# Optimization experiments

Measured on AMD Instinct MI355X. Metric: run time of the kernel, lower is better.

Reference implementation:

```python
import jax, jax.numpy as jnp
import numpy as np

B, H, L, N = 8, 128, 4096, 64
EPS = 1e-7
LOG_DT_MIN, LOG_DT_MAX = np.log(0.001), np.log(0.1)


def setup_inputs() -> dict:
    key = jax.random.key(0)
    k_u, k_lre, k_w, k_step = jax.random.split(key, 4)
    u = jax.random.normal(k_u, (B, H, L), dtype=jnp.float32)
    # HiPPO-style diagonal init: Re(Lambda) < 0 for stability, Im(Lambda) = pi*n
    Lambda_re = -0.5 * jnp.ones((H, N), jnp.float32) \
        - 0.1 * jax.random.uniform(k_lre, (H, N), dtype=jnp.float32)
    Lambda_im = jnp.broadcast_to(jnp.pi * jnp.arange(N, dtype=jnp.float32), (H, N))
    # W stored as (real, imag) pairs, stddev sqrt(0.5) per the module's initializer
    W_ri = (0.5 ** 0.5) * jax.random.normal(k_w, (H, N, 2), dtype=jnp.float32)
    D = jnp.ones((H,), jnp.float32)
    # log_step ~ U[log(1e-3), log(1e-1)] per log_step_initializer
    log_step = jax.random.uniform(k_step, (H,), dtype=jnp.float32) \
        * (LOG_DT_MAX - LOG_DT_MIN) + LOG_DT_MIN
    return {"u": u, "Lambda_re": Lambda_re, "Lambda_im": Lambda_im,
            "W_ri": W_ri, "D": D, "log_step": log_step}


def _dss_kernel(W, Lambda, step, Lseq):
    # P[h,n,l] = step_h * Lambda_hn * l
    pos = jnp.arange(Lseq, dtype=jnp.float32)
    P = (step[:, None] * Lambda)[..., None] * pos          # [H,N,L] complex64
    # complex softmax over l, stabilized by the entry with largest real part
    idx = jnp.argmax(P.real, axis=-1)[..., None]           # [H,N,1]
    e = jnp.exp(P - jnp.take_along_axis(P, idx, axis=-1))
    s = jnp.sum(e, axis=-1, keepdims=True)
    S = e * (jnp.conj(s) / (s * jnp.conj(s) + EPS))        # e / s, eps-regularized
    return jnp.einsum('hn,hnl->hl', W / Lambda, S).real    # [H,L]


def reference(u, Lambda_re, Lambda_im, W_ri, D, log_step):
    Lambda = Lambda_re + 1j * Lambda_im                    # [H,N]
    W = W_ri[..., 0] + 1j * W_ri[..., 1]                   # [H,N]
    step = jnp.exp(log_step)                               # [H]
    Lseq = u.shape[-1]
    K = _dss_kernel(W, Lambda, step, Lseq)                 # [H,L]
    # FFT-based causal convolution, zero-padded to 2L
    n = 2 * Lseq
    uf = jnp.fft.rfft(u, n=n, axis=-1)                     # [B,H,L+1]
    Kf = jnp.fft.rfft(K, n=n, axis=-1)                     # [H,L+1]
    y = jnp.fft.irfft(uf * Kf[None], n=n, axis=-1)[..., :Lseq]
    return y + D[None, :, None] * u
```

## Files before the change

kernel.cpp:

```cpp
#include <hip/hip_runtime.h>
#include <math.h>

#define H_  128
#define N_  64
#define L_  4096
#define B_  8
#define LC  128
#define NCH 32

typedef _Float16 f16;
typedef _Float16 half8 __attribute__((ext_vector_type(8)));
typedef _Float16 f16x4 __attribute__((ext_vector_type(4)));
typedef _Float16 f16x2 __attribute__((ext_vector_type(2)));
typedef float    floatx4 __attribute__((ext_vector_type(4)));

#define WS_T 0
#define WS_G ((size_t)H_*LC*LC*2)
#define WS_M ((size_t)2*H_*LC*LC*2)
#define WS_Q ((size_t)3*H_*LC*LC*2)

__device__ __forceinline__ float fexp(float x) {
    return __builtin_amdgcn_exp2f(x * 1.4426950408889634f);
}
__device__ __forceinline__ void fcis(float th, float& cs, float& sn) {
    double rev = (double)th * 0.15915494309189535;
    rev -= floor(rev);
    const float r = (float)rev;
    sn = __builtin_amdgcn_sinf(r);
    cs = __builtin_amdgcn_cosf(r);
}
__device__ __forceinline__ void fcis64(double th, float& cs, float& sn) {
    double rev = th * 0.15915494309189535;
    rev -= floor(rev);
    const float r = (float)rev;
    sn = __builtin_amdgcn_sinf(r);
    cs = __builtin_amdgcn_cosf(r);
}

__device__ __forceinline__ void dss_consts(int h, int n,
    const float* __restrict__ Lre, const float* __restrict__ Lim,
    const float* __restrict__ Wri, const float* __restrict__ lstep,
    float& af, float& bf, float& crf, float& cif, float& qrf, float& qif)
{
    const float stepf = fexp(lstep[h]);
    const float a  = stepf * Lre[h*N_ + n];
    const float bp = stepf * Lim[h*N_ + n];
    const float em = fexp(a);
    float rcs, rsn; fcis(bp, rcs, rsn);
    const float rre = em*rcs, rim = em*rsn;
    const float eL = fexp(a * 4096.0f);
    float cL, sL; fcis64((double)bp * 4096.0, cL, sL);
    const float rLre = eL*cL, rLim = eL*sL;
    const float nre = 1.0f - rLre, nim = -rLim;
    const float dre = 1.0f - rre,  dim = -rim;
    const float dm  = dre*dre + dim*dim;
    const float sre = (nre*dre + nim*dim) / dm;
    const float sim = (nim*dre - nre*dim) / dm;
    const float wre = Wri[(h*N_ + n)*2 + 0];
    const float wim = Wri[(h*N_ + n)*2 + 1];
    const float lre = Lre[h*N_ + n], lim = Lim[h*N_ + n];
    const float lm  = lre*lre + lim*lim;
    const float wor = (wre*lre + wim*lim) / lm;
    const float woi = (wim*lre - wre*lim) / lm;
    const float sm  = sre*sre + sim*sim + 1e-7f;
    crf = (wor*sre + woi*sim) / sm;
    cif = (woi*sre - wor*sim) / sm;
    const float eC = fexp(a * 128.0f);
    float cC, sC; fcis64((double)bp * 128.0, cC, sC);
    qrf = eC*cC; qif = eC*sC;
    af = a; bf = bp;
}

__global__ __launch_bounds__(256)
void dss_prep(const float* __restrict__ Lre, const float* __restrict__ Lim,
              const float* __restrict__ Wri, const float* __restrict__ Dv,
              const float* __restrict__ lstep, char* __restrict__ ws)
{
    __shared__ float s_a[N_], s_b[N_], s_cr[N_], s_ci[N_];
    __shared__ float sKp[2][128];
    __shared__ float sK[128];
    const int h = blockIdx.x;
    const int which = blockIdx.y;
    const int t = threadIdx.x;

    if (t < N_) {
        float a, b, cr, ci, qr, qi;
        dss_consts(h, t, Lre, Lim, Wri, lstep, a, b, cr, ci, qr, qi);
        s_a[t] = a; s_b[t] = b; s_cr[t] = cr; s_ci[t] = ci;
        if (which == 0) {
            float* qg = (float*)(ws + WS_Q) + (size_t)h*N_*2;
            qg[2*t] = qr; qg[2*t+1] = qi;
        }
    }
    __syncthreads();

    if (which == 0) {
        const int lag = t & 127, hf = t >> 7;
        float acc = 0.f;
        #pragma unroll
        for (int m = 0; m < 32; ++m) {
            const int n = hf*32 + m;
            const float ex = fexp(s_a[n] * (float)lag);
            float cs, sn; fcis(s_b[n] * (float)lag, cs, sn);
            acc = fmaf(ex, s_cr[n]*cs - s_ci[n]*sn, acc);
        }
        sKp[hf][lag] = acc;
        __syncthreads();
        if (t < 128) {
            float kv = sKp[0][t] + sKp[1][t];
            if (t == 0) kv += Dv[h];
            sK[t] = kv;
        }
        __syncthreads();
        f16* Tg = (f16*)(ws + WS_T) + (size_t)h*LC*LC;
        #pragma unroll
        for (int i = 0; i < 8; ++i) {
            const int e8 = t + i*256;
            const int row = e8 >> 4, c0 = (e8 & 15) * 8;
            half8 pv;
            #pragma unroll
            for (int j = 0; j < 8; ++j) {
                const int col = c0 + j;
                pv[j] = (f16)((row >= col) ? sK[row - col] : 0.f);
            }
            *reinterpret_cast<half8*>(&Tg[row*LC + c0]) = pv;
        }
    } else if (which == 1) {
        f16* Gg = (f16*)(ws + WS_G) + (size_t)h*LC*LC;
        #pragma unroll
        for (int i = 0; i < 8; ++i) {
            const int e8 = t + i*256;
            const int row = e8 >> 4, c0 = (e8 & 15) * 8;
            const int m = row >> 1, im = row & 1;
            const float a = s_a[m], b = s_b[m];
            half8 pv;
            #pragma unroll
            for (int j = 0; j < 8; ++j) {
                const float p = (float)(127 - (c0 + j));
                const float ex = fexp(a * p);
                float cs, sn; fcis(b * p, cs, sn);
                pv[j] = (f16)(im ? ex*sn : ex*cs);
            }
            *reinterpret_cast<half8*>(&Gg[row*LC + c0]) = pv;
        }
    } else {
        f16* Mg = (f16*)(ws + WS_M) + (size_t)h*LC*LC;
        #pragma unroll
        for (int i = 0; i < 8; ++i) {
            const int e8 = t + i*256;
            const int row = e8 >> 4, c0 = (e8 & 15) * 8;
            const float p = (float)(row + 1);
            half8 pv;
            #pragma unroll
            for (int mm = 0; mm < 4; ++mm) {
                const int m = (c0 >> 1) + mm;
                const float ex = fexp(s_a[m] * p);
                float cs, sn; fcis(s_b[m] * p, cs, sn);
                const float pr = ex*cs, pi = ex*sn;
                pv[2*mm]   = (f16)( 16.f * (s_cr[m]*pr - s_ci[m]*pi));
                pv[2*mm+1] = (f16)(-16.f * (s_cr[m]*pi + s_ci[m]*pr));
            }
            *reinterpret_cast<half8*>(&Mg[row*LC + c0]) = pv;
        }
    }
}

__global__ __launch_bounds__(256, 4)
void dss_main(const float* __restrict__ u, const char* __restrict__ ws,
              float* __restrict__ out)
{
    __shared__ f16   sU[NCH][132];
    __shared__ float sE[NCH][132];
    __shared__ f16   sC[NCH][132];

    const int t  = threadIdx.x;
    const int bh = blockIdx.x;
    const int h  = bh & (H_-1);
    const f16* Tg = (const f16*)(ws + WS_T) + (size_t)h*LC*LC;
    const f16* Gg = (const f16*)(ws + WS_G) + (size_t)h*LC*LC;
    const f16* Mg = (const f16*)(ws + WS_M) + (size_t)h*LC*LC;
    const float* qg = (const float*)(ws + WS_Q) + (size_t)h*N_*2;

    {
        const float4* up = reinterpret_cast<const float4*>(u + (size_t)bh * L_);
        #pragma unroll
        for (int i = 0; i < L_/4/256; ++i) {
            const int e4 = t + i*256;
            const float4 v = up[e4];
            const int row = e4 >> 5, c4 = (e4 & 31) * 4;
            f16x4 pv = { (f16)v.x, (f16)v.y, (f16)v.z, (f16)v.w };
            *reinterpret_cast<f16x4*>(&sU[row][c4]) = pv;
        }
    }
    __syncthreads();

    const int w  = t >> 6;
    const int l  = t & 63;
    const int lr = l & 15;
    const int lg = l >> 4;

    floatx4 accA[2][2] = {};
    floatx4 accB[2][2] = {};

    #pragma unroll
    for (int ks = 0; ks < 4; ++ks) {
        const int ko = ks*32 + lg*8;
        const half8 a0 = *reinterpret_cast<const half8*>(&sU[lr     ][ko]);
        const half8 a1 = *reinterpret_cast<const half8*>(&sU[16 + lr][ko]);
        #pragma unroll
        for (int nt = 0; nt < 2; ++nt) {
            const int ncol = (2*w + nt)*16 + lr;
            const half8 bT = *reinterpret_cast<const half8*>(&Tg[ncol*LC + ko]);
            const half8 bG = *reinterpret_cast<const half8*>(&Gg[ncol*LC + ko]);
            accA[0][nt] = __builtin_amdgcn_mfma_f32_16x16x32_f16(a0, bT, accA[0][nt], 0, 0, 0);
            accA[1][nt] = __builtin_amdgcn_mfma_f32_16x16x32_f16(a1, bT, accA[1][nt], 0, 0, 0);
            accB[0][nt] = __builtin_amdgcn_mfma_f32_16x16x32_f16(a0, bG, accB[0][nt], 0, 0, 0);
            accB[1][nt] = __builtin_amdgcn_mfma_f32_16x16x32_f16(a1, bG, accB[1][nt], 0, 0, 0);
        }
    }
    #pragma unroll
    for (int mt = 0; mt < 2; ++mt)
        #pragma unroll
        for (int nt = 0; nt < 2; ++nt)
            #pragma unroll
            for (int j = 0; j < 4; ++j)
                sE[mt*16 + lg*4 + j][(2*w + nt)*16 + lr] = accB[mt][nt][j];
    __syncthreads();

    if (w == 0) {
        const float qre = qg[2*l], qim = qg[2*l+1];
        float cr = 0.f, ci = 0.f;
        #pragma unroll
        for (int gb = 0; gb < 4; ++gb) {
            float2 E[8];
            #pragma unroll
            for (int j = 0; j < 8; ++j)
                E[j] = *reinterpret_cast<const float2*>(&sE[gb*8 + j][2*l]);
            #pragma unroll
            for (int j = 0; j < 8; ++j) {
                *reinterpret_cast<f16x2*>(&sC[gb*8 + j][2*l]) =
                    (f16x2){ (f16)(cr * 0.0625f), (f16)(ci * 0.0625f) };
                const float ncr = fmaf(qre, cr, fmaf(-qim, ci, E[j].x));
                const float nci = fmaf(qre, ci, fmaf( qim, cr, E[j].y));
                cr = ncr; ci = nci;
            }
        }
    }
    __syncthreads();

    #pragma unroll
    for (int ks = 0; ks < 4; ++ks) {
        const int ko = ks*32 + lg*8;
        const half8 a0 = *reinterpret_cast<const half8*>(&sC[lr     ][ko]);
        const half8 a1 = *reinterpret_cast<const half8*>(&sC[16 + lr][ko]);
        #pragma unroll
        for (int nt = 0; nt < 2; ++nt) {
            const int ncol = (2*w + nt)*16 + lr;
            const half8 bM = *reinterpret_cast<const half8*>(&Mg[ncol*LC + ko]);
            accA[0][nt] = __builtin_amdgcn_mfma_f32_16x16x32_f16(a0, bM, accA[0][nt], 0, 0, 0);
            accA[1][nt] = __builtin_amdgcn_mfma_f32_16x16x32_f16(a1, bM, accA[1][nt], 0, 0, 0);
        }
    }

    #pragma unroll
    for (int mt = 0; mt < 2; ++mt)
        #pragma unroll
        for (int nt = 0; nt < 2; ++nt)
            #pragma unroll
            for (int j = 0; j < 4; ++j)
                sE[mt*16 + lg*4 + j][(2*w + nt)*16 + lr] = accA[mt][nt][j];
    __syncthreads();
    {
        float4* op = reinterpret_cast<float4*>(out + (size_t)bh * L_);
        #pragma unroll
        for (int i = 0; i < L_/4/256; ++i) {
            const int e4 = t + i*256;
            const int row = e4 >> 5, c4 = (e4 & 31) * 4;
            op[e4] = *reinterpret_cast<const float4*>(&sE[row][c4]);
        }
    }
}

extern "C" void kernel_launch(void* const* d_in, const int* in_sizes, int n_in,
                              void* d_out, int out_size, void* d_ws, size_t ws_size,
                              hipStream_t stream) {
    const float* u  = (const float*)d_in[0];
    const float* lr = (const float*)d_in[1];
    const float* li = (const float*)d_in[2];
    const float* w  = (const float*)d_in[3];
    const float* dv = (const float*)d_in[4];
    const float* ls = (const float*)d_in[5];
    float* out = (float*)d_out;
    char* ws = (char*)d_ws;
    dss_prep<<<dim3(H_, 3), dim3(256), 0, stream>>>(lr, li, w, dv, ls, ws);
    dss_main<<<dim3(B_*H_), dim3(256), 0, stream>>>(u, ws, out);
}
```

Measured before the change: 96.30 us.

## Fuse prep into main kernel, build matrices in registers, two batches per block

After: 95.35 us. About the same (-1.0%).

```diff
diff --git a/kernel.cpp b/kernel.cpp
--- a/kernel.cpp
+++ b/kernel.cpp
@@ -7,17 +7,13 @@
 #define B_  8
 #define LC  128
 #define NCH 32
+#define TPB 512
 
 typedef _Float16 f16;
 typedef _Float16 half8 __attribute__((ext_vector_type(8)));
 typedef _Float16 f16x4 __attribute__((ext_vector_type(4)));
 typedef _Float16 f16x2 __attribute__((ext_vector_type(2)));
 typedef float    floatx4 __attribute__((ext_vector_type(4)));
-
-#define WS_T 0
-#define WS_G ((size_t)H_*LC*LC*2)
-#define WS_M ((size_t)2*H_*LC*LC*2)
-#define WS_Q ((size_t)3*H_*LC*LC*2)
 
 __device__ __forceinline__ float fexp(float x) {
     return __builtin_amdgcn_exp2f(x * 1.4426950408889634f);
@@ -37,64 +33,62 @@
     cs = __builtin_amdgcn_cosf(r);
 }
 
-__device__ __forceinline__ void dss_consts(int h, int n,
-    const float* __restrict__ Lre, const float* __restrict__ Lim,
-    const float* __restrict__ Wri, const float* __restrict__ lstep,
-    float& af, float& bf, float& crf, float& cif, float& qrf, float& qif)
+__global__ __launch_bounds__(TPB, 4)
+void dss_one(const float* __restrict__ u,
+             const float* __restrict__ Lre, const float* __restrict__ Lim,
+             const float* __restrict__ Wri, const float* __restrict__ Dv,
+             const float* __restrict__ lstep, float* __restrict__ out)
 {
-    const float stepf = fexp(lstep[h]);
-    const float a  = stepf * Lre[h*N_ + n];
-    const float bp = stepf * Lim[h*N_ + n];
-    const float em = fexp(a);
-    float rcs, rsn; fcis(bp, rcs, rsn);
-    const float rre = em*rcs, rim = em*rsn;
-    const float eL = fexp(a * 4096.0f);
-    float cL, sL; fcis64((double)bp * 4096.0, cL, sL);
-    const float rLre = eL*cL, rLim = eL*sL;
-    const float nre = 1.0f - rLre, nim = -rLim;
-    const float dre = 1.0f - rre,  dim = -rim;
-    const float dm  = dre*dre + dim*dim;
-    const float sre = (nre*dre + nim*dim) / dm;
-    const float sim = (nim*dre - nre*dim) / dm;
-    const float wre = Wri[(h*N_ + n)*2 + 0];
-    const float wim = Wri[(h*N_ + n)*2 + 1];
-    const float lre = Lre[h*N_ + n], lim = Lim[h*N_ + n];
-    const float lm  = lre*lre + lim*lim;
-    const float wor = (wre*lre + wim*lim) / lm;
-    const float woi = (wim*lre - wre*lim) / lm;
-    const float sm  = sre*sre + sim*sim + 1e-7f;
-    crf = (wor*sre + woi*sim) / sm;
-    cif = (woi*sre - wor*sim) / sm;
-    const float eC = fexp(a * 128.0f);
-    float cC, sC; fcis64((double)bp * 128.0, cC, sC);
-    qrf = eC*cC; qif = eC*sC;
-    af = a; bf = bp;
-}
-
-__global__ __launch_bounds__(256)
-void dss_prep(const float* __restrict__ Lre, const float* __restrict__ Lim,
-              const float* __restrict__ Wri, const float* __restrict__ Dv,
-              const float* __restrict__ lstep, char* __restrict__ ws)
-{
-    __shared__ float s_a[N_], s_b[N_], s_cr[N_], s_ci[N_];
-    __shared__ float sKp[2][128];
-    __shared__ float sK[128];
-    const int h = blockIdx.x;
-    const int which = blockIdx.y;
+    __shared__ f16   sU[NCH][132];
+    __shared__ float sE[NCH][132];
+    __shared__ f16   sC[NCH][132];
+    __shared__ float sKp[2][LC];
+    __shared__ float sK[LC];
+    __shared__ float s_a[N_], s_b[N_], s_cr[N_], s_ci[N_], sQ[2*N_];
+
     const int t = threadIdx.x;
+    const int h = blockIdx.x & (H_-1);
+    const int s = blockIdx.x >> 7;
+
+    float4 p0, p1;
+    {
+        const float4* up = reinterpret_cast<const float4*>(u + ((size_t)(2*s)*H_ + h) * L_);
+        p0 = up[t]; p1 = up[t + TPB];
+    }
 
     if (t < N_) {
-        float a, b, cr, ci, qr, qi;
-        dss_consts(h, t, Lre, Lim, Wri, lstep, a, b, cr, ci, qr, qi);
-        s_a[t] = a; s_b[t] = b; s_cr[t] = cr; s_ci[t] = ci;
-        if (which == 0) {
-            float* qg = (float*)(ws + WS_Q) + (size_t)h*N_*2;
-            qg[2*t] = qr; qg[2*t+1] = qi;
-        }
+        const int n = t;
+        const float stepf = fexp(lstep[h]);
+        const float a  = stepf * Lre[h*N_ + n];
+        const float bp = stepf * Lim[h*N_ + n];
+        const float em = fexp(a);
+        float rcs, rsn; fcis(bp, rcs, rsn);
+        const float rre = em*rcs, rim = em*rsn;
+        const float eL = fexp(a * 4096.0f);
+        float cL, sL; fcis64((double)bp * 4096.0, cL, sL);
+        const float rLre = eL*cL, rLim = eL*sL;
+        const float nre = 1.0f - rLre, nim = -rLim;
+        const float dre = 1.0f - rre,  dim = -rim;
+        const float dm  = dre*dre + dim*dim;
+        const float sre = (nre*dre + nim*dim) / dm;
+        const float sim = (nim*dre - nre*dim) / dm;
+        const float wre = Wri[(h*N_ + n)*2 + 0];
+        const float wim = Wri[(h*N_ + n)*2 + 1];
+        const float lre = Lre[h*N_ + n], lim = Lim[h*N_ + n];
+        const float lm  = lre*lre + lim*lim;
+        const float wor = (wre*lre + wim*lim) / lm;
+        const float woi = (wim*lre - wre*lim) / lm;
+        const float sm  = sre*sre + sim*sim + 1e-7f;
+        s_a[n] = a; s_b[n] = bp;
+        s_cr[n] = (wor*sre + woi*sim) / sm;
+        s_ci[n] = (woi*sre - wor*sim) / sm;
+        const float eC = fexp(a * 128.0f);
+        float cC, sC2; fcis64((double)bp * 128.0, cC, sC2);
+        sQ[2*n] = eC*cC; sQ[2*n+1] = eC*sC2;
     }
     __syncthreads();
 
-    if (which == 0) {
+    if (t < 256) {
         const int lag = t & 127, hf = t >> 7;
         float acc = 0.f;
         #pragma unroll
@@ -105,92 +99,12 @@
             acc = fmaf(ex, s_cr[n]*cs - s_ci[n]*sn, acc);
         }
         sKp[hf][lag] = acc;
-        __syncthreads();
-        if (t < 128) {
-            float kv = sKp[0][t] + sKp[1][t];
-            if (t == 0) kv += Dv[h];
-            sK[t] = kv;
-        }
-        __syncthreads();
-        f16* Tg = (f16*)(ws + WS_T) + (size_t)h*LC*LC;
-        #pragma unroll
-        for (int i = 0; i < 8; ++i) {
-            const int e8 = t + i*256;
-            const int row = e8 >> 4, c0 = (e8 & 15) * 8;
-            half8 pv;
-            #pragma unroll
-            for (int j = 0; j < 8; ++j) {
-                const int col = c0 + j;
-                pv[j] = (f16)((row >= col) ? sK[row - col] : 0.f);
-            }
-            *reinterpret_cast<half8*>(&Tg[row*LC + c0]) = pv;
-        }
-    } else if (which == 1) {
-        f16* Gg = (f16*)(ws + WS_G) + (size_t)h*LC*LC;
-        #pragma unroll
-        for (int i = 0; i < 8; ++i) {
-            const int e8 = t + i*256;
-            const int row = e8 >> 4, c0 = (e8 & 15) * 8;
-            const int m = row >> 1, im = row & 1;
-            const float a = s_a[m], b = s_b[m];
-            half8 pv;
-            #pragma unroll
-            for (int j = 0; j < 8; ++j) {
-                const float p = (float)(127 - (c0 + j));
-                const float ex = fexp(a * p);
-                float cs, sn; fcis(b * p, cs, sn);
-                pv[j] = (f16)(im ? ex*sn : ex*cs);
-            }
-            *reinterpret_cast<half8*>(&Gg[row*LC + c0]) = pv;
-        }
-    } else {
-        f16* Mg = (f16*)(ws + WS_M) + (size_t)h*LC*LC;
-        #pragma unroll
-        for (int i = 0; i < 8; ++i) {
-            const int e8 = t + i*256;
-            const int row = e8 >> 4, c0 = (e8 & 15) * 8;
-            const float p = (float)(row + 1);
-            half8 pv;
-            #pragma unroll
-            for (int mm = 0; mm < 4; ++mm) {
-                const int m = (c0 >> 1) + mm;
-                const float ex = fexp(s_a[m] * p);
-                float cs, sn; fcis(s_b[m] * p, cs, sn);
-                const float pr = ex*cs, pi = ex*sn;
-                pv[2*mm]   = (f16)( 16.f * (s_cr[m]*pr - s_ci[m]*pi));
-                pv[2*mm+1] = (f16)(-16.f * (s_cr[m]*pi + s_ci[m]*pr));
-            }
-            *reinterpret_cast<half8*>(&Mg[row*LC + c0]) = pv;
-        }
-    }
-}
-
-__global__ __launch_bounds__(256, 4)
-void dss_main(const float* __restrict__ u, const char* __restrict__ ws,
-              float* __restrict__ out)
-{
-    __shared__ f16   sU[NCH][132];
-    __shared__ float sE[NCH][132];
-    __shared__ f16   sC[NCH][132];
-
-    const int t  = threadIdx.x;
-    const int bh = blockIdx.x;
-    const int h  = bh & (H_-1);
-    const f16* Tg = (const f16*)(ws + WS_T) + (size_t)h*LC*LC;
-    const f16* Gg = (const f16*)(ws + WS_G) + (size_t)h*LC*LC;
-    const f16* Mg = (const f16*)(ws + WS_M) + (size_t)h*LC*LC;
-    const float* qg = (const float*)(ws + WS_Q) + (size_t)h*N_*2;
-
-    {
-        const float4* up = reinterpret_cast<const float4*>(u + (size_t)bh * L_);
-        #pragma unroll
-        for (int i = 0; i < L_/4/256; ++i) {
-            const int e4 = t + i*256;
-            const float4 v = up[e4];
-            const int row = e4 >> 5, c4 = (e4 & 31) * 4;
-            f16x4 pv = { (f16)v.x, (f16)v.y, (f16)v.z, (f16)v.w };
-            *reinterpret_cast<f16x4*>(&sU[row][c4]) = pv;
-        }
+    }
+    __syncthreads();
+    if (t < LC) {
+        float kv = sKp[0][t] + sKp[1][t];
+        if (t == 0) kv += Dv[h];
+        sK[t] = kv;
     }
     __syncthreads();
 
@@ -198,86 +112,122 @@
     const int l  = t & 63;
     const int lr = l & 15;
     const int lg = l >> 4;
-
-    floatx4 accA[2][2] = {};
-    floatx4 accB[2][2] = {};
+    const int pos = w*16 + lr;
+
+    half8 bT[4], bG[4], bM[4];
+    {
+        const int   gm  = pos >> 1, gim = pos & 1;
+        const float ga  = s_a[gm],  gb  = s_b[gm];
+        const float pm  = (float)(pos + 1);
+        #pragma unroll
+        for (int ks = 0; ks < 4; ++ks) {
+            const int ko = ks*32 + lg*8;
+            #pragma unroll
+            for (int j = 0; j < 8; ++j) {
+                const int col = ko + j;
+                bT[ks][j] = (f16)((pos >= col) ? sK[pos - col] : 0.f);
+            }
+            #pragma unroll
+            for (int j = 0; j < 8; ++j) {
+                const float p = (float)(127 - (ko + j));
+                const float ex = fexp(ga * p);
+                float cs, sn; fcis(gb * p, cs, sn);
+                bG[ks][j] = (f16)(gim ? ex*sn : ex*cs);
+            }
+            #pragma unroll
+            for (int mm = 0; mm < 4; ++mm) {
+                const int m = (ko >> 1) + mm;
+                const float ex = fexp(s_a[m] * pm);
+                float cs, sn; fcis(s_b[m] * pm, cs, sn);
+                const float pr = ex*cs, pi = ex*sn;
+                bM[ks][2*mm]   = (f16)( 16.f * (s_cr[m]*pr - s_ci[m]*pi));
+                bM[ks][2*mm+1] = (f16)(-16.f * (s_cr[m]*pi + s_ci[m]*pr));
+            }
+        }
+    }
 
     #pragma unroll
-    for (int ks = 0; ks < 4; ++ks) {
-        const int ko = ks*32 + lg*8;
-        const half8 a0 = *reinterpret_cast<const half8*>(&sU[lr     ][ko]);
-        const half8 a1 = *reinterpret_cast<const half8*>(&sU[16 + lr][ko]);
-        #pragma unroll
-        for (int nt = 0; nt < 2; ++nt) {
-            const int ncol = (2*w + nt)*16 + lr;
-            const half8 bT = *reinterpret_cast<const half8*>(&Tg[ncol*LC + ko]);
-            const half8 bG = *reinterpret_cast<const half8*>(&Gg[ncol*LC + ko]);
-            accA[0][nt] = __builtin_amdgcn_mfma_f32_16x16x32_f16(a0, bT, accA[0][nt], 0, 0, 0);
-            accA[1][nt] = __builtin_amdgcn_mfma_f32_16x16x32_f16(a1, bT, accA[1][nt], 0, 0, 0);
-            accB[0][nt] = __builtin_amdgcn_mfma_f32_16x16x32_f16(a0, bG, accB[0][nt], 0, 0, 0);
-            accB[1][nt] = __builtin_amdgcn_mfma_f32_16x16x32_f16(a1, bG, accB[1][nt], 0, 0, 0);
-        }
-    }
-    #pragma unroll
-    for (int mt = 0; mt < 2; ++mt)
-        #pragma unroll
-        for (int nt = 0; nt < 2; ++nt)
+    for (int i = 0; i < 2; ++i) {
+        #pragma unroll
+        for (int j = 0; j < 2; ++j) {
+            const float4 v = j ? p1 : p0;
+            const int e4 = t + j*TPB;
+            const int row = e4 >> 5, c4 = (e4 & 31) * 4;
+            f16x4 pv = { (f16)v.x, (f16)v.y, (f16)v.z, (f16)v.w };
+            *reinterpret_cast<f16x4*>(&sU[row][c4]) = pv;
+        }
+        if (i == 0) {
+            const float4* up = reinterpret_cast<const float4*>(u + ((size_t)(2*s+1)*H_ + h) * L_);
+            p0 = up[t]; p1 = up[t + TPB];
+        }
+        __syncthreads();
+
+        floatx4 accA[2] = {};
+        floatx4 accB[2] = {};
+
+        #pragma unroll
+        for (int ks = 0; ks < 4; ++ks) {
+            const int ko = ks*32 + lg*8;
+            const half8 a0 = *reinterpret_cast<const half8*>(&sU[lr     ][ko]);
+            const half8 a1 = *reinterpret_cast<const half8*>(&sU[16 + lr][ko]);
+            accA[0] = __builtin_amdgcn_mfma_f32_16x16x32_f16(a0, bT[ks], accA[0], 0, 0, 0);
+            accA[1] = __builtin_amdgcn_mfma_f32_16x16x32_f16(a1, bT[ks], accA[1], 0, 0, 0);
+            accB[0] = __builtin_amdgcn_mfma_f32_16x16x32_f16(a0, bG[ks], accB[0], 0, 0, 0);
+            accB[1] = __builtin_amdgcn_mfma_f32_16x16x32_f16(a1, bG[ks], accB[1], 0, 0, 0);
+        }
+        #pragma unroll
+        for (int mt = 0; mt < 2; ++mt)
             #pragma unroll
             for (int j = 0; j < 4; ++j)
-                sE[mt*16 + lg*4 + j][(2*w + nt)*16 + lr] = accB[mt][nt][j];
-    __syncthreads();
-
-    if (w == 0) {
-        const float qre = qg[2*l], qim = qg[2*l+1];
-        float cr = 0.f, ci = 0.f;
-        #pragma unroll
-        for (int gb = 0; gb < 4; ++gb) {
-            float2 E[8];
-            #pragma unroll
-            for (int j = 0; j < 8; ++j)
-                E[j] = *reinterpret_cast<const float2*>(&sE[gb*8 + j][2*l]);
-            #pragma unroll
-            for (int j = 0; j < 8; ++j) {
-                *reinterpret_cast<f16x2*>(&sC[gb*8 + j][2*l]) =
-                    (f16x2){ (f16)(cr * 0.0625f), (f16)(ci * 0.0625f) };
-                const float ncr = fmaf(qre, cr, fmaf(-qim, ci, E[j].x));
-                const float nci = fmaf(qre, ci, fmaf( qim, cr, E[j].y));
-                cr = ncr; ci = nci;
-            }
-        }
-    }
-    __syncthreads();
-
-    #pragma unroll
-    for (int ks = 0; ks < 4; ++ks) {
-        const int ko = ks*32 + lg*8;
-        const half8 a0 = *reinterpret_cast<const half8*>(&sC[lr     ][ko]);
-        const half8 a1 = *reinterpret_cast<const half8*>(&sC[16 + lr][ko]);
-        #pragma unroll
-        for (int nt = 0; nt < 2; ++nt) {
-            const int ncol = (2*w + nt)*16 + lr;
-            const half8 bM = *reinterpret_cast<const half8*>(&Mg[ncol*LC + ko]);
-            accA[0][nt] = __builtin_amdgcn_mfma_f32_16x16x32_f16(a0, bM, accA[0][nt], 0, 0, 0);
-            accA[1][nt] = __builtin_amdgcn_mfma_f32_16x16x32_f16(a1, bM, accA[1][nt], 0, 0, 0);
-        }
-    }
-
-    #pragma unroll
-    for (int mt = 0; mt < 2; ++mt)
-        #pragma unroll
-        for (int nt = 0; nt < 2; ++nt)
+                sE[mt*16 + lg*4 + j][pos] = accB[mt][j];
+        __syncthreads();
+
+        if (w == 0) {
+            const float qre = sQ[2*l], qim = sQ[2*l+1];
+            float cr = 0.f, ci = 0.f;
+            #pragma unroll
+            for (int gb = 0; gb < 4; ++gb) {
+                float2 E[8];
+                #pragma unroll
+                for (int j = 0; j < 8; ++j)
+                    E[j] = *reinterpret_cast<const float2*>(&sE[gb*8 + j][2*l]);
+                #pragma unroll
+                for (int j = 0; j < 8; ++j) {
+                    *reinterpret_cast<f16x2*>(&sC[gb*8 + j][2*l]) =
+                        (f16x2){ (f16)(cr * 0.0625f), (f16)(ci * 0.0625f) };
+                    const float ncr = fmaf(qre, cr, fmaf(-qim, ci, E[j].x));
+                    const float nci = fmaf(qre, ci, fmaf( qim, cr, E[j].y));
+                    cr = ncr; ci = nci;
+                }
+            }
+        }
+        __syncthreads();
+
+        #pragma unroll
+        for (int ks = 0; ks < 4; ++ks) {
+            const int ko = ks*32 + lg*8;
+            const half8 a0 = *reinterpret_cast<const half8*>(&sC[lr     ][ko]);
+            const half8 a1 = *reinterpret_cast<const half8*>(&sC[16 + lr][ko]);
+            accA[0] = __builtin_amdgcn_mfma_f32_16x16x32_f16(a0, bM[ks], accA[0], 0, 0, 0);
+            accA[1] = __builtin_amdgcn_mfma_f32_16x16x32_f16(a1, bM[ks], accA[1], 0, 0, 0);
+        }
+        #pragma unroll
+        for (int mt = 0; mt < 2; ++mt)
             #pragma unroll
             for (int j = 0; j < 4; ++j)
-                sE[mt*16 + lg*4 + j][(2*w + nt)*16 + lr] = accA[mt][nt][j];
-    __syncthreads();
-    {
-        float4* op = reinterpret_cast<float4*>(out + (size_t)bh * L_);
-        #pragma unroll
-        for (int i = 0; i < L_/4/256; ++i) {
-            const int e4 = t + i*256;
-            const int row = e4 >> 5, c4 = (e4 & 31) * 4;
-            op[e4] = *reinterpret_cast<const float4*>(&sE[row][c4]);
-        }
+                sE[mt*16 + lg*4 + j][pos] = accA[mt][j];
+        __syncthreads();
+
+        {
+            float4* op = reinterpret_cast<float4*>(out + ((size_t)(2*s + i)*H_ + h) * L_);
+            #pragma unroll
+            for (int j = 0; j < 2; ++j) {
+                const int e4 = t + j*TPB;
+                const int row = e4 >> 5, c4 = (e4 & 31) * 4;
+                op[e4] = *reinterpret_cast<const float4*>(&sE[row][c4]);
+            }
+        }
+        __syncthreads();
     }
 }
 
@@ -291,7 +241,5 @@
     const float* dv = (const float*)d_in[4];
     const float* ls = (const float*)d_in[5];
     float* out = (float*)d_out;
-    char* ws = (char*)d_ws;
-    dss_prep<<<dim3(H_, 3), dim3(256), 0, stream>>>(lr, li, w, dv, ls, ws);
-    dss_main<<<dim3(B_*H_), dim3(256), 0, stream>>>(u, ws, out);
-}
+    dss_one<<<dim3(H_*4), dim3(TPB), 0, stream>>>(u, lr, li, w, dv, ls, out);
+}
```
